# Optimization experiments

Measured on AMD Instinct MI355X. Metric: run time of the kernel, lower is better.

Reference implementation:

```python
import jax, jax.numpy as jnp
import numpy as np

B, T, L, W = 4, 4096, 64, 8          # batch, text len, media tokens, max_window_per_audio
DIM, DIM_A, H, DH = 2048, 1024, 8, 64
INNER = H * DH
LN_EPS = 1e-5


def setup_inputs() -> dict:
    key = jax.random.key(0)
    ks = jax.random.split(key, 8)
    x = jax.random.normal(ks[0], (B, T, DIM), jnp.float32)
    media = jax.random.normal(ks[1], (B, L, 1, DIM_A), jnp.float32)
    media_mask = jax.random.uniform(ks[2], (B, L, 1)) > 0.1
    # sparse media markers (~8 per row); ensure at least one per row
    media_locations = (jax.random.uniform(ks[3], (B, T)) < (8.0 / T)).astype(jnp.int32)
    media_locations = media_locations.at[:, 0].set(1)
    Wq = jax.random.normal(ks[4], (DIM, INNER), jnp.float32) / np.sqrt(DIM).astype(np.float32)
    Wkv = jax.random.normal(ks[5], (DIM_A, 2 * INNER), jnp.float32) / np.sqrt(DIM_A).astype(np.float32)
    Wout = jax.random.normal(ks[6], (INNER, DIM), jnp.float32) / np.sqrt(INNER).astype(np.float32)
    gamma = jnp.ones((DIM,), jnp.float32)
    beta = jnp.zeros((DIM,), jnp.float32)
    return dict(x=x, media=media, media_mask=media_mask, media_locations=media_locations,
                Wq=Wq, Wkv=Wkv, Wout=Wout, gamma=gamma, beta=beta)


def reference(x, media, media_mask, media_locations, Wq, Wkv, Wout, gamma, beta):
    scale = DH ** -0.5
    # LayerNorm (biased variance, like torch)
    mu = x.mean(-1, keepdims=True)
    var = x.var(-1, keepdims=True)
    xn = (x - mu) * jax.lax.rsqrt(var + LN_EPS) * gamma + beta
    # projections
    q = (xn @ Wq).reshape(B, T, H, DH).transpose(0, 2, 1, 3) * scale   # [B,h,T,dh]
    kv = media.reshape(B, L, DIM_A) @ Wkv
    k, v = jnp.split(kv, 2, axis=-1)
    k = k.reshape(B, L, H, DH).transpose(0, 2, 1, 3)                   # [B,h,L,dh]
    v = v.reshape(B, L, H, DH).transpose(0, 2, 1, 3)
    sim = jnp.einsum('bhid,bhjd->bhij', q, k)                          # [B,h,T,L]
    big = jnp.finfo(sim.dtype).max
    # media validity mask
    mm = media_mask.reshape(B, 1, 1, L)
    sim = jnp.where(mm, sim, -big)
    # few-shot window mask (only_attend_immediate_media=False):
    # token t attends windows [0, max(#media at <=t, 1) * W)
    cum = jnp.cumsum((media_locations != 0).astype(jnp.int32), axis=1)  # [B,T]
    end = jnp.maximum(cum, 1) * W                                       # [B,T]
    fsm = jnp.arange(L)[None, None, :] < end[:, :, None]                # [B,T,L]
    sim = jnp.where(fsm[:, None], sim, -big)
    sim = sim - jax.lax.stop_gradient(sim.max(-1, keepdims=True))
    attn = jax.nn.softmax(sim, axis=-1)
    out = jnp.einsum('bhij,bhjd->bhid', attn, v)                        # [B,h,T,dh]
    out = out.transpose(0, 2, 1, 3).reshape(B, T, INNER)
    return out @ Wout
```

## Files before the change

### kernel.cpp

```cpp
#include <hip/hip_runtime.h>
#include <float.h>

typedef __bf16 bf16;
typedef __bf16 bf16x8 __attribute__((ext_vector_type(8)));
typedef float f32x4 __attribute__((ext_vector_type(4)));

#define GAS __attribute__((address_space(1)))
#define LAS __attribute__((address_space(3)))

__device__ __forceinline__ void gload_lds16(const void* g, void* l) {
  __builtin_amdgcn_global_load_lds((const GAS unsigned int*)g, (LAS unsigned int*)l, 16, 0, 0);
}

__global__ __launch_bounds__(256, 2) void qattn(
    const bf16* __restrict__ xn, const bf16* __restrict__ wqT,
    const bf16* __restrict__ kvb, const int* __restrict__ mk,
    const int* __restrict__ endw, bf16* __restrict__ aob) {
  constexpr int K = 2048;
  __shared__ __align__(16) bf16 Abuf[2][128 * 64];
  __shared__ __align__(16) bf16 Bbuf[2][128 * 64];
  const int tid = threadIdx.x, lane = tid & 63;
  const int w = tid >> 6, wr = w >> 1, wc = w & 1;
  const int g = lane >> 4, fr = lane & 15;

  const int gx = gridDim.x;
  int lid = blockIdx.y * gx + blockIdx.x;
  lid = ((lid & 7) << 6) | (lid >> 3);
  const int bx = lid % gx, by = lid / gx;
  const size_t m0 = (size_t)by * 128;
  const int n0 = bx * 128;
  const int b = by >> 5;

  const int nt = K >> 6;
  const int srow = tid >> 3, sslot = tid & 7;

  f32x4 acc[4][4] = {};

  auto stage = [&](int t) {
    const int s = t & 1;
    const int kt = t << 6;
#pragma unroll
    for (int c = 0; c < 4; ++c) {
      const int r = c * 32 + srow;
      gload_lds16(xn + (m0 + r) * (size_t)K + kt + ((sslot ^ (r & 7)) << 3),
                  &Abuf[s][c * 2048 + w * 512]);
    }
#pragma unroll
    for (int c = 0; c < 4; ++c) {
      const int r = c * 32 + srow;
      gload_lds16(wqT + (size_t)(n0 + r) * K + kt + ((sslot ^ (r & 7)) << 3),
                  &Bbuf[s][c * 2048 + w * 512]);
    }
  };
  auto rdA = [&](int s, int mi, int ks) {
    const int r = wr * 64 + mi * 16 + fr;
    return *(const bf16x8*)&Abuf[s][r * 64 + ((((ks << 2) | g) ^ (r & 7)) << 3)];
  };
  auto rdB = [&](int s, int ni, int ks) {
    const int r = wc * 64 + ni * 16 + fr;
    return *(const bf16x8*)&Bbuf[s][r * 64 + ((((ks << 2) | g) ^ (r & 7)) << 3)];
  };
  auto compute = [&](int t) {
    const int s = t & 1;
    bf16x8 bv[4][2];
#pragma unroll
    for (int ni = 0; ni < 4; ++ni)
#pragma unroll
      for (int ks = 0; ks < 2; ++ks) bv[ni][ks] = rdB(s, ni, ks);
    __builtin_amdgcn_s_setprio(1);
#pragma unroll
    for (int mi = 0; mi < 4; ++mi)
#pragma unroll
      for (int ks = 0; ks < 2; ++ks) {
        const bf16x8 av = rdA(s, mi, ks);
#pragma unroll
        for (int ni = 0; ni < 4; ++ni)
          acc[mi][ni] = __builtin_amdgcn_mfma_f32_16x16x32_bf16(
              av, bv[ni][ks], acc[mi][ni], 0, 0, 0);
      }
    __builtin_amdgcn_s_setprio(0);
  };

  stage(0);
  for (int t = 0; t < nt; ++t) {
    __syncthreads();
    if (t + 1 < nt) stage(t + 1);
    compute(t);
  }

  __syncthreads();

  bf16* QP = &Abuf[0][0] + w * 4096;
  bf16* Klds = &Bbuf[0][0];
  bf16* Vlds = &Bbuf[1][0];

#pragma unroll
  for (int mi = 0; mi < 4; ++mi)
#pragma unroll
    for (int ni = 0; ni < 4; ++ni)
#pragma unroll
      for (int rg = 0; rg < 4; ++rg) {
        const int row = mi * 16 + g * 4 + rg, col = ni * 16 + fr;
        QP[row * 64 + (((col >> 3) ^ (row & 7)) << 3) + (col & 7)] =
            (bf16)acc[mi][ni][rg];
      }

#pragma unroll
  for (int j = 0; j < 4; ++j) {
    const int idx = j * 256 + tid;
    const int head = idx >> 9, l = (idx >> 3) & 63, sl = idx & 7;
    gload_lds16(kvb + (size_t)(b * 64 + l) * 1024 + (2 * bx + head) * 64 +
                    ((sl ^ (l & 7)) << 3),
                Klds + (j * 256 + w * 64) * 8);
  }
#pragma unroll
  for (int j = 0; j < 4; ++j) {
    const int idx = j * 256 + tid;
    const int head = idx >> 9, l = (idx >> 3) & 63, sg = idx & 7;
    bf16x8 vv = *(const bf16x8*)&kvb[(size_t)(b * 64 + l) * 1024 + 512 +
                                     (2 * bx + head) * 64 + sg * 8];
#pragma unroll
    for (int e = 0; e < 8; ++e) {
      const int dh = sg * 8 + e;
      Vlds[head * 4096 + dh * 64 + (((l >> 3) ^ (dh & 7)) << 3) + (l & 7)] =
          vv[e];
    }
  }
  asm volatile("s_waitcnt vmcnt(0)" ::: "memory");
  __syncthreads();

  f32x4 sacc[4][4] = {};
#pragma unroll
  for (int ks = 0; ks < 2; ++ks) {
    bf16x8 aq[4], bk[4];
#pragma unroll
    for (int mi = 0; mi < 4; ++mi) {
      const int r = mi * 16 + fr;
      aq[mi] = *(const bf16x8*)&QP[r * 64 + ((((ks << 2) | g) ^ (r & 7)) << 3)];
    }
#pragma unroll
    for (int ni = 0; ni < 4; ++ni) {
      const int l = ni * 16 + fr;
      bk[ni] = *(const bf16x8*)&Klds[wc * 4096 + l * 64 +
                                     ((((ks << 2) | g) ^ (l & 7)) << 3)];
    }
#pragma unroll
    for (int mi = 0; mi < 4; ++mi)
#pragma unroll
      for (int ni = 0; ni < 4; ++ni)
        sacc[mi][ni] = __builtin_amdgcn_mfma_f32_16x16x32_bf16(
            aq[mi], bk[ni], sacc[mi][ni], 0, 0, 0);
  }

#pragma unroll
  for (int mi = 0; mi < 4; ++mi) {
    const int4 ev4 = *(const int4*)&endw[m0 + wr * 64 + mi * 16 + g * 4];
    const int ev[4] = {ev4.x, ev4.y, ev4.z, ev4.w};
    float p[4][4];
#pragma unroll
    for (int ni = 0; ni < 4; ++ni) {
      const int l = ni * 16 + fr;
      const bool mv = (mk[b * 64 + l] != 0);
#pragma unroll
      for (int rg = 0; rg < 4; ++rg)
        p[ni][rg] = (mv && (l < ev[rg])) ? sacc[mi][ni][rg] : -FLT_MAX;
    }
#pragma unroll
    for (int rg = 0; rg < 4; ++rg) {
      float m = fmaxf(fmaxf(p[0][rg], p[1][rg]), fmaxf(p[2][rg], p[3][rg]));
      m = fmaxf(m, __shfl_xor(m, 1));
      m = fmaxf(m, __shfl_xor(m, 2));
      m = fmaxf(m, __shfl_xor(m, 4));
      m = fmaxf(m, __shfl_xor(m, 8));
      float sum = 0.f;
#pragma unroll
      for (int ni = 0; ni < 4; ++ni) {
        p[ni][rg] = __expf(p[ni][rg] - m);
        sum += p[ni][rg];
      }
      sum += __shfl_xor(sum, 1);
      sum += __shfl_xor(sum, 2);
      sum += __shfl_xor(sum, 4);
      sum += __shfl_xor(sum, 8);
      const float inv = 1.f / sum;
#pragma unroll
      for (int ni = 0; ni < 4; ++ni) p[ni][rg] *= inv;
    }
#pragma unroll
    for (int ni = 0; ni < 4; ++ni) {
      const int l = ni * 16 + fr;
#pragma unroll
      for (int rg = 0; rg < 4; ++rg) {
        const int row = mi * 16 + g * 4 + rg;
        QP[row * 64 + (((l >> 3) ^ (row & 7)) << 3) + (l & 7)] =
            (bf16)p[ni][rg];
      }
    }
  }

  f32x4 oacc[4][4] = {};
#pragma unroll
  for (int ks = 0; ks < 2; ++ks) {
    bf16x8 pa[4], bv[4];
#pragma unroll
    for (int mi = 0; mi < 4; ++mi) {
      const int r = mi * 16 + fr;
      pa[mi] = *(const bf16x8*)&QP[r * 64 + ((((ks << 2) | g) ^ (r & 7)) << 3)];
    }
#pragma unroll
    for (int nd = 0; nd < 4; ++nd) {
      const int dh = nd * 16 + fr;
      bv[nd] = *(const bf16x8*)&Vlds[wc * 4096 + dh * 64 +
                                     ((((ks << 2) | g) ^ (dh & 7)) << 3)];
    }
#pragma unroll
    for (int mi = 0; mi < 4; ++mi)
#pragma unroll
      for (int nd = 0; nd < 4; ++nd)
        oacc[mi][nd] = __builtin_amdgcn_mfma_f32_16x16x32_bf16(
            pa[mi], bv[nd], oacc[mi][nd], 0, 0, 0);
  }
#pragma unroll
  for (int mi = 0; mi < 4; ++mi)
#pragma unroll
    for (int nd = 0; nd < 4; ++nd)
#pragma unroll
      for (int rg = 0; rg < 4; ++rg) {
        const size_t t = m0 + wr * 64 + mi * 16 + g * 4 + rg;
        aob[t * 512 + (2 * bx + wc) * 64 + nd * 16 + fr] =
            (bf16)oacc[mi][nd][rg];
      }
}

template <int OUT_BF16>
__global__ __launch_bounds__(256, 2) void gemm_bt(
    const bf16* __restrict__ A, const bf16* __restrict__ Bt,
    void* __restrict__ Cv, int M, int N, int K) {
  __shared__ bf16 As[128 * 32];
  __shared__ bf16 Bs[128 * 32];
  const int tid = threadIdx.x;
  const int lane = tid & 63, w = tid >> 6;
  const int wr = w >> 1, wc = w & 1;

  const int gx = gridDim.x;
  const int nwg = gx * gridDim.y;
  int lid = blockIdx.y * gx + blockIdx.x;
  {
    const int qq = nwg >> 3, rr = nwg & 7;
    const int xcd = lid & 7, pos = lid >> 3;
    lid = (xcd < rr ? xcd * (qq + 1) : rr * (qq + 1) + (xcd - rr) * qq) + pos;
  }
  const int bx = lid % gx, by = lid / gx;
  const size_t m0 = (size_t)by * 128, n0 = (size_t)bx * 128;

  const int srow = lane >> 2, sslot = lane & 3;
  const int g = lane >> 4, fr = lane & 15;

  f32x4 acc[4][4] = {};

  for (int kt = 0; kt < K; kt += 32) {
    __syncthreads();
#pragma unroll
    for (int j = 0; j < 2; ++j) {
      const int c = 2 * w + j;
      const int r = c * 16 + srow;
      const int ks = (sslot ^ (r & 3)) << 3;
      gload_lds16(A + (m0 + r) * K + kt + ks, &As[c * 512]);
      gload_lds16(Bt + (n0 + r) * K + kt + ks, &Bs[c * 512]);
    }
    __syncthreads();
    bf16x8 av[4], bv[4];
#pragma unroll
    for (int mi = 0; mi < 4; ++mi) {
      const int r = wr * 64 + mi * 16 + fr;
      av[mi] = *(const bf16x8*)&As[r * 32 + ((g ^ (r & 3)) << 3)];
    }
#pragma unroll
    for (int ni = 0; ni < 4; ++ni) {
      const int r = wc * 64 + ni * 16 + fr;
      bv[ni] = *(const bf16x8*)&Bs[r * 32 + ((g ^ (r & 3)) << 3)];
    }
#pragma unroll
    for (int mi = 0; mi < 4; ++mi)
#pragma unroll
      for (int ni = 0; ni < 4; ++ni)
        acc[mi][ni] = __builtin_amdgcn_mfma_f32_16x16x32_bf16(
            av[mi], bv[ni], acc[mi][ni], 0, 0, 0);
  }

#pragma unroll
  for (int mi = 0; mi < 4; ++mi)
#pragma unroll
    for (int ni = 0; ni < 4; ++ni)
#pragma unroll
      for (int rg = 0; rg < 4; ++rg) {
        const size_t row = m0 + wr * 64 + mi * 16 + g * 4 + rg;
        const size_t col = n0 + wc * 64 + ni * 16 + fr;
        if (OUT_BF16)
          ((bf16*)Cv)[row * (size_t)N + col] = (bf16)acc[mi][ni][rg];
        else
          ((float*)Cv)[row * (size_t)N + col] = acc[mi][ni][rg];
      }
}

__device__ __forceinline__ void transp64(const float* __restrict__ src,
                                         bf16* __restrict__ dst, int R, int C,
                                         float scale, int tile, float* lds) {
  const int tilesC = C >> 6;
  const int tr = tile / tilesC, tc = tile % tilesC;
  const int r0 = tr << 6, c0 = tc << 6;
  const int tid = threadIdx.x;
  const int lr = tid >> 6, lc = tid & 63;
#pragma unroll
  for (int j = 0; j < 16; ++j) {
    const int r = j * 4 + lr;
    lds[r * 65 + lc] = src[(size_t)(r0 + r) * C + c0 + lc];
  }
  __syncthreads();
#pragma unroll
  for (int j = 0; j < 16; ++j) {
    const int rr = j * 4 + lr;
    dst[(size_t)(c0 + rr) * R + r0 + lc] = (bf16)(lds[lc * 65 + rr] * scale);
  }
}

__global__ __launch_bounds__(256) void prep_all(
    const float* __restrict__ x, const float* __restrict__ gamma,
    const float* __restrict__ beta, bf16* __restrict__ xn,
    const float* __restrict__ Wq, bf16* __restrict__ wqT,
    const float* __restrict__ Wkv, bf16* __restrict__ wkvT,
    const float* __restrict__ Wout, bf16* __restrict__ woT,
    const float* __restrict__ media, bf16* __restrict__ medb,
    const int* __restrict__ mloc, int* __restrict__ endw,
    const unsigned char* __restrict__ mraw, int* __restrict__ mk) {
  __shared__ float shf[64 * 65];
  const int blk = blockIdx.x, tid = threadIdx.x;

  if (blk < 16384) {
    const size_t base = (size_t)blk * 2048 + tid * 8;
    f32x4 v0 = *(const f32x4*)(x + base);
    f32x4 v1 = *(const f32x4*)(x + base + 4);
    float s = 0.f, q2 = 0.f;
#pragma unroll
    for (int j = 0; j < 4; ++j) {
      s += v0[j] + v1[j];
      q2 += v0[j] * v0[j] + v1[j] * v1[j];
    }
    for (int off = 32; off > 0; off >>= 1) {
      s += __shfl_down(s, off);
      q2 += __shfl_down(q2, off);
    }
    const int lane = tid & 63, wv = tid >> 6;
    if (lane == 0) { shf[wv] = s; shf[4 + wv] = q2; }
    __syncthreads();
    s = shf[0] + shf[1] + shf[2] + shf[3];
    q2 = shf[4] + shf[5] + shf[6] + shf[7];
    const float mu = s * (1.f / 2048.f);
    const float var = q2 * (1.f / 2048.f) - mu * mu;
    const float rs = rsqrtf(var + 1e-5f);
    f32x4 g0 = *(const f32x4*)(gamma + tid * 8);
    f32x4 g1 = *(const f32x4*)(gamma + tid * 8 + 4);
    f32x4 b0 = *(const f32x4*)(beta + tid * 8);
    f32x4 b1 = *(const f32x4*)(beta + tid * 8 + 4);
    bf16x8 o;
#pragma unroll
    for (int j = 0; j < 4; ++j) {
      o[j] = (bf16)((v0[j] - mu) * rs * g0[j] + b0[j]);
      o[4 + j] = (bf16)((v1[j] - mu) * rs * g1[j] + b1[j]);
    }
    *(bf16x8*)(xn + base) = o;
  } else if (blk < 16640) {
    transp64(Wq, wqT, 2048, 512, 0.125f, blk - 16384, shf);
  } else if (blk < 16896) {
    transp64(Wkv, wkvT, 1024, 1024, 1.f, blk - 16640, shf);
  } else if (blk < 17152) {
    transp64(Wout, woT, 512, 2048, 1.f, blk - 16896, shf);
  } else if (blk < 18176) {
    const int i = (blk - 17152) * 256 + tid;
    medb[i] = (bf16)media[i];
  } else if (blk < 18180) {
    int* part = (int*)shf;
    const int b = blk - 18176;
    int loc[16];
    int s = 0;
    const int base = b * 4096 + tid * 16;
#pragma unroll
    for (int j = 0; j < 16; ++j) {
      loc[j] = (mloc[base + j] != 0) ? 1 : 0;
      s += loc[j];
    }
    part[tid] = s;
    __syncthreads();
    for (int off = 1; off < 256; off <<= 1) {
      int v = (tid >= off) ? part[tid - off] : 0;
      __syncthreads();
      part[tid] += v;
      __syncthreads();
    }
    int c = (tid > 0) ? part[tid - 1] : 0;
#pragma unroll
    for (int j = 0; j < 16; ++j) {
      c += loc[j];
      int e = (c > 1 ? c : 1) << 3;
      endw[base + j] = e > 64 ? 64 : e;
    }
  } else {
    int* isbool = (int*)shf;
    if (tid == 0) *isbool = 0;
    __syncthreads();
    const unsigned char v = mraw[tid];
    if ((tid & 3) != 0 && v != 0) atomicOr(isbool, 1);
    __syncthreads();
    mk[tid] = (*isbool) ? (int)mraw[tid] : ((const int*)mraw)[tid];
  }
}

extern "C" void kernel_launch(void* const* d_in, const int* in_sizes, int n_in,
                              void* d_out, int out_size, void* d_ws,
                              size_t ws_size, hipStream_t stream) {
  const float* x = (const float*)d_in[0];
  const float* media = (const float*)d_in[1];
  const unsigned char* mraw = (const unsigned char*)d_in[2];
  const int* mloc = (const int*)d_in[3];
  const float* Wq = (const float*)d_in[4];
  const float* Wkv = (const float*)d_in[5];
  const float* Wout = (const float*)d_in[6];
  const float* gamma = (const float*)d_in[7];
  const float* beta = (const float*)d_in[8];
  float* out = (float*)d_out;

  bf16* xn = (bf16*)d_out;

  char* ws = (char*)d_ws;
  size_t off = 0;
  auto carve = [&](size_t bytes) {
    void* p = ws + off;
    off += (bytes + 255) & ~(size_t)255;
    return p;
  };
  bf16* aob = (bf16*)carve((size_t)16384 * 512 * 2);
  bf16* kvb = (bf16*)carve((size_t)256 * 1024 * 2);
  bf16* wqT = (bf16*)carve((size_t)512 * 2048 * 2);
  bf16* wkvT = (bf16*)carve((size_t)1024 * 1024 * 2);
  bf16* woT = (bf16*)carve((size_t)2048 * 512 * 2);
  bf16* medb = (bf16*)carve((size_t)256 * 1024 * 2);
  int* endw = (int*)carve((size_t)4 * 4096 * 4);
  int* mk = (int*)carve(256 * 4);
  (void)ws_size;
  (void)in_sizes;
  (void)n_in;
  (void)out_size;

  prep_all<<<18181, 256, 0, stream>>>(x, gamma, beta, xn, Wq, wqT, Wkv, wkvT,
                                      Wout, woT, media, medb, mloc, endw, mraw,
                                      mk);

  gemm_bt<1><<<dim3(8, 2), 256, 0, stream>>>(medb, wkvT, kvb, 256, 1024, 1024);

  qattn<<<dim3(4, 128), 256, 0, stream>>>(xn, wqT, kvb, mk, endw, aob);

  gemm_bt<0><<<dim3(16, 128), 256, 0, stream>>>(aob, woT, out, 16384, 2048,
                                                512);
}
```

Baseline: 162.0 us.

## Fuse media KV projection GEMM into prep kernel, drop Wkv transpose and media cast

Computes the media@Wkv projection directly inside the prep kernel in 16 blocks placed first in the grid. Each block reads the fp32 media and Wkv, converts them to bf16 on the fly into swizzled LDS tiles, and runs MFMA. This removes the separate gemm launch, the Wkv transpose blocks and the media cast blocks, along with their intermediate buffers. The fused GEMM blocks use a single buffer, do uncoalesced scalar LDS stores for B, and hold 128x128 tiles over K=1024. They may run long enough to become a tail inside the prep kernel.

```diff
diff --git a/kernel.cpp b/kernel.cpp
--- a/kernel.cpp
+++ b/kernel.cpp
@@ -328,16 +328,82 @@
     const float* __restrict__ x, const float* __restrict__ gamma,
     const float* __restrict__ beta, bf16* __restrict__ xn,
     const float* __restrict__ Wq, bf16* __restrict__ wqT,
-    const float* __restrict__ Wkv, bf16* __restrict__ wkvT,
+    const float* __restrict__ Wkv, bf16* __restrict__ kvb,
     const float* __restrict__ Wout, bf16* __restrict__ woT,
-    const float* __restrict__ media, bf16* __restrict__ medb,
-    const int* __restrict__ mloc, int* __restrict__ endw,
-    const unsigned char* __restrict__ mraw, int* __restrict__ mk) {
+    const float* __restrict__ media, const int* __restrict__ mloc,
+    int* __restrict__ endw, const unsigned char* __restrict__ mraw,
+    int* __restrict__ mk) {
   __shared__ float shf[64 * 65];
   const int blk = blockIdx.x, tid = threadIdx.x;
 
-  if (blk < 16384) {
-    const size_t base = (size_t)blk * 2048 + tid * 8;
+  if (blk < 16) {
+    bf16* As = (bf16*)shf;
+    bf16* Bs = (bf16*)shf + 4096;
+    const int m0k = (blk >> 3) * 128, n0k = (blk & 7) * 128;
+    const int lane = tid & 63, w = tid >> 6;
+    const int wr = w >> 1, wc = w & 1;
+    const int g = lane >> 4, fr = lane & 15;
+    f32x4 acc[4][4] = {};
+    for (int kt = 0; kt < 1024; kt += 32) {
+      __syncthreads();
+#pragma unroll
+      for (int j = 0; j < 2; ++j) {
+        const int u = j * 256 + tid;
+        const int r = u >> 2, sl = u & 3;
+        const float* src = media + (size_t)(m0k + r) * 1024 + kt + sl * 8;
+        f32x4 v0 = *(const f32x4*)src;
+        f32x4 v1 = *(const f32x4*)(src + 4);
+        bf16x8 o;
+#pragma unroll
+        for (int e = 0; e < 4; ++e) {
+          o[e] = (bf16)v0[e];
+          o[4 + e] = (bf16)v1[e];
+        }
+        *(bf16x8*)&As[r * 32 + ((sl ^ (r & 3)) << 3)] = o;
+      }
+#pragma unroll
+      for (int j = 0; j < 4; ++j) {
+        const int u = j * 256 + tid;
+        const int kk = u >> 5, n4 = (u & 31) * 4;
+        f32x4 v = *(const f32x4*)(Wkv + (size_t)(kt + kk) * 1024 + n0k + n4);
+#pragma unroll
+        for (int e = 0; e < 4; ++e) {
+          const int n = n4 + e;
+          Bs[n * 32 + (((kk >> 3) ^ (n & 3)) << 3) + (kk & 7)] = (bf16)v[e];
+        }
+      }
+      __syncthreads();
+      bf16x8 av[4], bv[4];
+#pragma unroll
+      for (int mi = 0; mi < 4; ++mi) {
+        const int r = wr * 64 + mi * 16 + fr;
+        av[mi] = *(const bf16x8*)&As[r * 32 + ((g ^ (r & 3)) << 3)];
+      }
+#pragma unroll
+      for (int ni = 0; ni < 4; ++ni) {
+        const int r = wc * 64 + ni * 16 + fr;
+        bv[ni] = *(const bf16x8*)&Bs[r * 32 + ((g ^ (r & 3)) << 3)];
+      }
+#pragma unroll
+      for (int mi = 0; mi < 4; ++mi)
+#pragma unroll
+        for (int ni = 0; ni < 4; ++ni)
+          acc[mi][ni] = __builtin_amdgcn_mfma_f32_16x16x32_bf16(
+              av[mi], bv[ni], acc[mi][ni], 0, 0, 0);
+    }
+#pragma unroll
+    for (int mi = 0; mi < 4; ++mi)
+#pragma unroll
+      for (int ni = 0; ni < 4; ++ni)
+#pragma unroll
+        for (int rg = 0; rg < 4; ++rg) {
+          const int row = m0k + wr * 64 + mi * 16 + g * 4 + rg;
+          const int col = n0k + wc * 64 + ni * 16 + fr;
+          kvb[(size_t)row * 1024 + col] = (bf16)acc[mi][ni][rg];
+        }
+  } else if (blk < 16400) {
+    const int row = blk - 16;
+    const size_t base = (size_t)row * 2048 + tid * 8;
     f32x4 v0 = *(const f32x4*)(x + base);
     f32x4 v1 = *(const f32x4*)(x + base + 4);
     float s = 0.f, q2 = 0.f;
@@ -369,18 +435,13 @@
       o[4 + j] = (bf16)((v1[j] - mu) * rs * g1[j] + b1[j]);
     }
     *(bf16x8*)(xn + base) = o;
-  } else if (blk < 16640) {
-    transp64(Wq, wqT, 2048, 512, 0.125f, blk - 16384, shf);
-  } else if (blk < 16896) {
-    transp64(Wkv, wkvT, 1024, 1024, 1.f, blk - 16640, shf);
-  } else if (blk < 17152) {
-    transp64(Wout, woT, 512, 2048, 1.f, blk - 16896, shf);
-  } else if (blk < 18176) {
-    const int i = (blk - 17152) * 256 + tid;
-    medb[i] = (bf16)media[i];
-  } else if (blk < 18180) {
+  } else if (blk < 16656) {
+    transp64(Wq, wqT, 2048, 512, 0.125f, blk - 16400, shf);
+  } else if (blk < 16912) {
+    transp64(Wout, woT, 512, 2048, 1.f, blk - 16656, shf);
+  } else if (blk < 16916) {
     int* part = (int*)shf;
-    const int b = blk - 18176;
+    const int b = blk - 16912;
     int loc[16];
     int s = 0;
     const int base = b * 4096 + tid * 16;
@@ -441,9 +502,7 @@
   bf16* aob = (bf16*)carve((size_t)16384 * 512 * 2);
   bf16* kvb = (bf16*)carve((size_t)256 * 1024 * 2);
   bf16* wqT = (bf16*)carve((size_t)512 * 2048 * 2);
-  bf16* wkvT = (bf16*)carve((size_t)1024 * 1024 * 2);
   bf16* woT = (bf16*)carve((size_t)2048 * 512 * 2);
-  bf16* medb = (bf16*)carve((size_t)256 * 1024 * 2);
   int* endw = (int*)carve((size_t)4 * 4096 * 4);
   int* mk = (int*)carve(256 * 4);
   (void)ws_size;
@@ -451,11 +510,8 @@
   (void)n_in;
   (void)out_size;
 
-  prep_all<<<18181, 256, 0, stream>>>(x, gamma, beta, xn, Wq, wqT, Wkv, wkvT,
-                                      Wout, woT, media, medb, mloc, endw, mraw,
-                                      mk);
-
-  gemm_bt<1><<<dim3(8, 2), 256, 0, stream>>>(medb, wkvT, kvb, 256, 1024, 1024);
+  prep_all<<<16917, 256, 0, stream>>>(x, gamma, beta, xn, Wq, wqT, Wkv, kvb,
+                                      Wout, woT, media, mloc, endw, mraw, mk);
 
   qattn<<<dim3(4, 128), 256, 0, stream>>>(xn, wqT, kvb, mk, endw, aob);
 
```

Measured after the change: 198.5 us. +22.6%, slower.

## Fuse KV projection GEMM into attention kernel with atomic completion flag

Applied to the files above, without the earlier changes.

Removes the separate small KV-projection GEMM launch and computes it inside the first 16 blocks of the attention kernel. Those blocks write kvb and bump a global counter, and every block spin-waits on the counter before loading K/V. This saves one kernel launch and its tail gap. In exchange it adds extra serial work to 16 blocks and creates a cross-block dependency that can deadlock if those blocks are not resident.

```diff
diff --git a/kernel.cpp b/kernel.cpp
--- a/kernel.cpp
+++ b/kernel.cpp
@@ -14,8 +14,10 @@
 
 __global__ __launch_bounds__(256, 2) void qattn(
     const bf16* __restrict__ xn, const bf16* __restrict__ wqT,
-    const bf16* __restrict__ kvb, const int* __restrict__ mk,
-    const int* __restrict__ endw, bf16* __restrict__ aob) {
+    const bf16* __restrict__ medb, const bf16* __restrict__ wkvT,
+    bf16* __restrict__ kvb, int* __restrict__ kvdone,
+    const int* __restrict__ mk, const int* __restrict__ endw,
+    bf16* __restrict__ aob) {
   constexpr int K = 2048;
   __shared__ __align__(16) bf16 Abuf[2][128 * 64];
   __shared__ __align__(16) bf16 Bbuf[2][128 * 64];
@@ -24,12 +26,64 @@
   const int g = lane >> 4, fr = lane & 15;
 
   const int gx = gridDim.x;
-  int lid = blockIdx.y * gx + blockIdx.x;
+  const int rid = blockIdx.y * gx + blockIdx.x;
+  int lid = rid;
   lid = ((lid & 7) << 6) | (lid >> 3);
   const int bx = lid % gx, by = lid / gx;
   const size_t m0 = (size_t)by * 128;
   const int n0 = bx * 128;
   const int b = by >> 5;
+
+  if (rid < 16) {
+    bf16* As = &Abuf[0][0];
+    bf16* Bs = &Abuf[0][0] + 4096;
+    const int m0k = (rid >> 3) * 128, n0k = (rid & 7) * 128;
+    const int srowk = lane >> 2, sslotk = lane & 3;
+    f32x4 acck[4][4] = {};
+    for (int kt = 0; kt < 1024; kt += 32) {
+      __syncthreads();
+#pragma unroll
+      for (int j = 0; j < 2; ++j) {
+        const int c = 2 * w + j;
+        const int r = c * 16 + srowk;
+        const int ks = (sslotk ^ (r & 3)) << 3;
+        gload_lds16(medb + (size_t)(m0k + r) * 1024 + kt + ks, &As[c * 512]);
+        gload_lds16(wkvT + (size_t)(n0k + r) * 1024 + kt + ks, &Bs[c * 512]);
+      }
+      __syncthreads();
+      bf16x8 av[4], bv[4];
+#pragma unroll
+      for (int mi = 0; mi < 4; ++mi) {
+        const int r = wr * 64 + mi * 16 + fr;
+        av[mi] = *(const bf16x8*)&As[r * 32 + ((g ^ (r & 3)) << 3)];
+      }
+#pragma unroll
+      for (int ni = 0; ni < 4; ++ni) {
+        const int r = wc * 64 + ni * 16 + fr;
+        bv[ni] = *(const bf16x8*)&Bs[r * 32 + ((g ^ (r & 3)) << 3)];
+      }
+#pragma unroll
+      for (int mi = 0; mi < 4; ++mi)
+#pragma unroll
+        for (int ni = 0; ni < 4; ++ni)
+          acck[mi][ni] = __builtin_amdgcn_mfma_f32_16x16x32_bf16(
+              av[mi], bv[ni], acck[mi][ni], 0, 0, 0);
+    }
+#pragma unroll
+    for (int mi = 0; mi < 4; ++mi)
+#pragma unroll
+      for (int ni = 0; ni < 4; ++ni)
+#pragma unroll
+        for (int rg = 0; rg < 4; ++rg) {
+          const int row = m0k + wr * 64 + mi * 16 + g * 4 + rg;
+          const int col = n0k + wc * 64 + ni * 16 + fr;
+          kvb[(size_t)row * 1024 + col] = (bf16)acck[mi][ni][rg];
+        }
+    __threadfence();
+    __syncthreads();
+    if (tid == 0) atomicAdd(kvdone, 1);
+    __syncthreads();
+  }
 
   const int nt = K >> 6;
   const int srow = tid >> 3, sslot = tid & 7;
@@ -105,6 +159,13 @@
             (bf16)acc[mi][ni][rg];
       }
 
+  if (tid == 0) {
+    while (__hip_atomic_load(kvdone, __ATOMIC_ACQUIRE,
+                             __HIP_MEMORY_SCOPE_AGENT) < 16) {
+    }
+  }
+  __syncthreads();
+
 #pragma unroll
   for (int j = 0; j < 4; ++j) {
     const int idx = j * 256 + tid;
@@ -332,7 +393,8 @@
     const float* __restrict__ Wout, bf16* __restrict__ woT,
     const float* __restrict__ media, bf16* __restrict__ medb,
     const int* __restrict__ mloc, int* __restrict__ endw,
-    const unsigned char* __restrict__ mraw, int* __restrict__ mk) {
+    const unsigned char* __restrict__ mraw, int* __restrict__ mk,
+    int* __restrict__ kvdone) {
   __shared__ float shf[64 * 65];
   const int blk = blockIdx.x, tid = threadIdx.x;
 
@@ -406,7 +468,10 @@
     }
   } else {
     int* isbool = (int*)shf;
-    if (tid == 0) *isbool = 0;
+    if (tid == 0) {
+      *isbool = 0;
+      *kvdone = 0;
+    }
     __syncthreads();
     const unsigned char v = mraw[tid];
     if ((tid & 3) != 0 && v != 0) atomicOr(isbool, 1);
@@ -446,6 +511,7 @@
   bf16* medb = (bf16*)carve((size_t)256 * 1024 * 2);
   int* endw = (int*)carve((size_t)4 * 4096 * 4);
   int* mk = (int*)carve(256 * 4);
+  int* kvdone = (int*)carve(256);
   (void)ws_size;
   (void)in_sizes;
   (void)n_in;
@@ -453,11 +519,10 @@
 
   prep_all<<<18181, 256, 0, stream>>>(x, gamma, beta, xn, Wq, wqT, Wkv, wkvT,
                                       Wout, woT, media, medb, mloc, endw, mraw,
-                                      mk);
-
-  gemm_bt<1><<<dim3(8, 2), 256, 0, stream>>>(medb, wkvT, kvb, 256, 1024, 1024);
-
-  qattn<<<dim3(4, 128), 256, 0, stream>>>(xn, wqT, kvb, mk, endw, aob);
+                                      mk, kvdone);
+
+  qattn<<<dim3(4, 128), 256, 0, stream>>>(xn, wqT, medb, wkvT, kvb, kvdone, mk,
+                                          endw, aob);
 
   gemm_bt<0><<<dim3(16, 128), 256, 0, stream>>>(aob, woT, out, 16384, 2048,
                                                 512);
```

Result: slower. 168.7 us (+4.1%).

## Prepack Wq in MFMA fragment order and triple-buffer A tiles in Q-GEMM

Applied to the files above, without the earlier changes.

Wq is now pre-packed in prep_all into the exact per-lane MFMA B-fragment layout, so the Q-projection loop reads B operands straight from global memory into registers instead of staging them through LDS. The A (normalized x) tiles move to a three-stage LDS ring with explicit vmcnt waits and a raw barrier, keeping loads two tiles ahead. This is meant to cut LDS traffic and barrier stalls in the main GEMM loop. In exchange, B fragments come from global or L2 on every tile, the packing kernel uses strided uncoalesced reads of Wq, and the hand-set vmcnt counts must stay in step with the number of outstanding loads.

```diff
diff --git a/kernel.cpp b/kernel.cpp
--- a/kernel.cpp
+++ b/kernel.cpp
@@ -12,13 +12,20 @@
   __builtin_amdgcn_global_load_lds((const GAS unsigned int*)g, (LAS unsigned int*)l, 16, 0, 0);
 }
 
+template <int N> struct ic { static constexpr int v = N; };
+template <int VM> __device__ __forceinline__ void wait_vmcnt() {
+  if constexpr (VM == 4) asm volatile("s_waitcnt vmcnt(4)" ::: "memory");
+  else if constexpr (VM == 8) asm volatile("s_waitcnt vmcnt(8)" ::: "memory");
+  else if constexpr (VM == 12) asm volatile("s_waitcnt vmcnt(12)" ::: "memory");
+}
+
 __global__ __launch_bounds__(256, 2) void qattn(
-    const bf16* __restrict__ xn, const bf16* __restrict__ wqT,
+    const bf16* __restrict__ xn, const bf16* __restrict__ wqTp,
     const bf16* __restrict__ kvb, const int* __restrict__ mk,
     const int* __restrict__ endw, bf16* __restrict__ aob) {
   constexpr int K = 2048;
-  __shared__ __align__(16) bf16 Abuf[2][128 * 64];
-  __shared__ __align__(16) bf16 Bbuf[2][128 * 64];
+  __shared__ __align__(16) bf16 Abuf[3][128 * 64];
+  __shared__ __align__(16) bf16 KV[2][128 * 64];
   const int tid = threadIdx.x, lane = tid & 63;
   const int w = tid >> 6, wr = w >> 1, wc = w & 1;
   const int g = lane >> 4, fr = lane & 15;
@@ -28,45 +35,43 @@
   lid = ((lid & 7) << 6) | (lid >> 3);
   const int bx = lid % gx, by = lid / gx;
   const size_t m0 = (size_t)by * 128;
-  const int n0 = bx * 128;
   const int b = by >> 5;
 
   const int nt = K >> 6;
   const int srow = tid >> 3, sslot = tid & 7;
+  const int cg = bx * 2 + wc;
+  const bf16* bpack = wqTp + (size_t)cg * 256 * 512 + lane * 8;
 
   f32x4 acc[4][4] = {};
 
-  auto stage = [&](int t) {
-    const int s = t & 1;
+  auto stageA = [&](int t) {
+    const int s = t % 3;
     const int kt = t << 6;
 #pragma unroll
     for (int c = 0; c < 4; ++c) {
       const int r = c * 32 + srow;
       gload_lds16(xn + (m0 + r) * (size_t)K + kt + ((sslot ^ (r & 7)) << 3),
                   &Abuf[s][c * 2048 + w * 512]);
-    }
-#pragma unroll
-    for (int c = 0; c < 4; ++c) {
-      const int r = c * 32 + srow;
-      gload_lds16(wqT + (size_t)(n0 + r) * K + kt + ((sslot ^ (r & 7)) << 3),
-                  &Bbuf[s][c * 2048 + w * 512]);
     }
   };
   auto rdA = [&](int s, int mi, int ks) {
     const int r = wr * 64 + mi * 16 + fr;
     return *(const bf16x8*)&Abuf[s][r * 64 + ((((ks << 2) | g) ^ (r & 7)) << 3)];
   };
-  auto rdB = [&](int s, int ni, int ks) {
-    const int r = wc * 64 + ni * 16 + fr;
-    return *(const bf16x8*)&Bbuf[s][r * 64 + ((((ks << 2) | g) ^ (r & 7)) << 3)];
-  };
-  auto compute = [&](int t) {
-    const int s = t & 1;
+
+  auto tile = [&](int t, auto vmtag, bool doStage) {
+    wait_vmcnt<decltype(vmtag)::v>();
+    __builtin_amdgcn_s_barrier();
+    __builtin_amdgcn_sched_barrier(0);
     bf16x8 bv[4][2];
-#pragma unroll
-    for (int ni = 0; ni < 4; ++ni)
-#pragma unroll
-      for (int ks = 0; ks < 2; ++ks) bv[ni][ks] = rdB(s, ni, ks);
+    const bf16* bp = bpack + (size_t)t * 8 * 512;
+#pragma unroll
+    for (int ks = 0; ks < 2; ++ks)
+#pragma unroll
+      for (int ni = 0; ni < 4; ++ni)
+        bv[ni][ks] = *(const bf16x8*)(bp + (ks * 4 + ni) * 512);
+    if (doStage) stageA(t + 2);
+    const int s = t % 3;
     __builtin_amdgcn_s_setprio(1);
 #pragma unroll
     for (int mi = 0; mi < 4; ++mi)
@@ -81,18 +86,17 @@
     __builtin_amdgcn_s_setprio(0);
   };
 
-  stage(0);
-  for (int t = 0; t < nt; ++t) {
-    __syncthreads();
-    if (t + 1 < nt) stage(t + 1);
-    compute(t);
-  }
+  stageA(0);
+  stageA(1);
+  tile(0, ic<4>{}, true);
+  for (int t = 1; t < nt - 1; ++t) tile(t, ic<12>{}, t + 2 < nt);
+  tile(nt - 1, ic<8>{}, false);
 
   __syncthreads();
 
   bf16* QP = &Abuf[0][0] + w * 4096;
-  bf16* Klds = &Bbuf[0][0];
-  bf16* Vlds = &Bbuf[1][0];
+  bf16* Klds = &KV[0][0];
+  bf16* Vlds = &KV[1][0];
 
 #pragma unroll
   for (int mi = 0; mi < 4; ++mi)
@@ -201,7 +205,7 @@
   f32x4 oacc[4][4] = {};
 #pragma unroll
   for (int ks = 0; ks < 2; ++ks) {
-    bf16x8 pa[4], bv[4];
+    bf16x8 pa[4], bvv[4];
 #pragma unroll
     for (int mi = 0; mi < 4; ++mi) {
       const int r = mi * 16 + fr;
@@ -210,15 +214,15 @@
 #pragma unroll
     for (int nd = 0; nd < 4; ++nd) {
       const int dh = nd * 16 + fr;
-      bv[nd] = *(const bf16x8*)&Vlds[wc * 4096 + dh * 64 +
-                                     ((((ks << 2) | g) ^ (dh & 7)) << 3)];
+      bvv[nd] = *(const bf16x8*)&Vlds[wc * 4096 + dh * 64 +
+                                      ((((ks << 2) | g) ^ (dh & 7)) << 3)];
     }
 #pragma unroll
     for (int mi = 0; mi < 4; ++mi)
 #pragma unroll
       for (int nd = 0; nd < 4; ++nd)
         oacc[mi][nd] = __builtin_amdgcn_mfma_f32_16x16x32_bf16(
-            pa[mi], bv[nd], oacc[mi][nd], 0, 0, 0);
+            pa[mi], bvv[nd], oacc[mi][nd], 0, 0, 0);
   }
 #pragma unroll
   for (int mi = 0; mi < 4; ++mi)
@@ -327,7 +331,7 @@
 __global__ __launch_bounds__(256) void prep_all(
     const float* __restrict__ x, const float* __restrict__ gamma,
     const float* __restrict__ beta, bf16* __restrict__ xn,
-    const float* __restrict__ Wq, bf16* __restrict__ wqT,
+    const float* __restrict__ Wq, bf16* __restrict__ wqTp,
     const float* __restrict__ Wkv, bf16* __restrict__ wkvT,
     const float* __restrict__ Wout, bf16* __restrict__ woT,
     const float* __restrict__ media, bf16* __restrict__ medb,
@@ -369,18 +373,28 @@
       o[4 + j] = (bf16)((v1[j] - mu) * rs * g1[j] + b1[j]);
     }
     *(bf16x8*)(xn + base) = o;
-  } else if (blk < 16640) {
-    transp64(Wq, wqT, 2048, 512, 0.125f, blk - 16384, shf);
   } else if (blk < 16896) {
-    transp64(Wkv, wkvT, 1024, 1024, 1.f, blk - 16640, shf);
+    const int chunk = (blk - 16384) * 4 + (tid >> 6);
+    const int l = tid & 63;
+    const int ni = chunk & 3, ks = (chunk >> 2) & 1;
+    const int t = (chunk >> 3) & 31, cgp = chunk >> 8;
+    const int n = cgp * 64 + ni * 16 + (l & 15);
+    const int kbase = t * 64 + (((ks << 2) | (l >> 4)) << 3);
+    bf16x8 o;
+#pragma unroll
+    for (int j = 0; j < 8; ++j)
+      o[j] = (bf16)(Wq[(size_t)(kbase + j) * 512 + n] * 0.125f);
+    *(bf16x8*)(wqTp + (size_t)chunk * 512 + l * 8) = o;
   } else if (blk < 17152) {
-    transp64(Wout, woT, 512, 2048, 1.f, blk - 16896, shf);
-  } else if (blk < 18176) {
-    const int i = (blk - 17152) * 256 + tid;
+    transp64(Wkv, wkvT, 1024, 1024, 1.f, blk - 16896, shf);
+  } else if (blk < 17408) {
+    transp64(Wout, woT, 512, 2048, 1.f, blk - 17152, shf);
+  } else if (blk < 18432) {
+    const int i = (blk - 17408) * 256 + tid;
     medb[i] = (bf16)media[i];
-  } else if (blk < 18180) {
+  } else if (blk < 18436) {
     int* part = (int*)shf;
-    const int b = blk - 18176;
+    const int b = blk - 18432;
     int loc[16];
     int s = 0;
     const int base = b * 4096 + tid * 16;
@@ -440,7 +454,7 @@
   };
   bf16* aob = (bf16*)carve((size_t)16384 * 512 * 2);
   bf16* kvb = (bf16*)carve((size_t)256 * 1024 * 2);
-  bf16* wqT = (bf16*)carve((size_t)512 * 2048 * 2);
+  bf16* wqTp = (bf16*)carve((size_t)512 * 2048 * 2);
   bf16* wkvT = (bf16*)carve((size_t)1024 * 1024 * 2);
   bf16* woT = (bf16*)carve((size_t)2048 * 512 * 2);
   bf16* medb = (bf16*)carve((size_t)256 * 1024 * 2);
@@ -451,13 +465,13 @@
   (void)n_in;
   (void)out_size;
 
-  prep_all<<<18181, 256, 0, stream>>>(x, gamma, beta, xn, Wq, wqT, Wkv, wkvT,
+  prep_all<<<18437, 256, 0, stream>>>(x, gamma, beta, xn, Wq, wqTp, Wkv, wkvT,
                                       Wout, woT, media, medb, mloc, endw, mraw,
                                       mk);
 
   gemm_bt<1><<<dim3(8, 2), 256, 0, stream>>>(medb, wkvT, kvb, 256, 1024, 1024);
 
-  qattn<<<dim3(4, 128), 256, 0, stream>>>(xn, wqT, kvb, mk, endw, aob);
+  qattn<<<dim3(4, 128), 256, 0, stream>>>(xn, wqTp, kvb, mk, endw, aob);
 
   gemm_bt<0><<<dim3(16, 128), 256, 0, stream>>>(aob, woT, out, 16384, 2048,
                                                 512);
```

After: 162.5 us. About the same (+0.3%).
